# Kernel optimization log

Hardware: AMD Instinct MI355X
Metric: run time of the kernel (lower is better)

The kernel has to match this reference:

```python
import jax, jax.numpy as jnp
import numpy as np

REG = 0.01
NUM_PS, NUM_QS, NUM_RS, D = 100000, 100000, 1000, 256
B = 4096


def setup_inputs() -> dict:
    key = jax.random.key(0)
    k1, k2, k3, k4, k5, k6, k7 = jax.random.split(key, 7)
    # xavier_uniform bound for a (d, d*d) fan view: sqrt(6/(d + d*d))
    bound = float(np.sqrt(6.0 / (D + D * D)))
    return {
        "ps": jax.random.randint(k1, (B,), 0, NUM_PS),
        "qs": jax.random.randint(k2, (B,), 0, NUM_QS),
        "rs": jax.random.randint(k3, (B,), 0, NUM_RS),
        "P_table": jax.random.normal(k4, (NUM_PS, D), dtype=jnp.float32),
        "Q_table": jax.random.normal(k5, (NUM_QS, D), dtype=jnp.float32),
        "R_table": jax.random.normal(k6, (NUM_RS, D), dtype=jnp.float32),
        "W": jax.random.uniform(k7, (D, D, D), dtype=jnp.float32, minval=-bound, maxval=bound),
    }


def reference(ps, qs, rs, P_table, Q_table, R_table, W):
    p = P_table[ps]  # (B, d)
    q = Q_table[qs]  # (B, d)
    r = R_table[rs]  # (B, d)
    # W.view(d, d*d) then reshape (B, d_r, d_q): axis order of W is (p, r, q)
    # trilinear: out_b = sum_{i,j,k} p_bi W_ijk r_bj q_bk
    Wp = jnp.einsum('bi,ijk->bjk', p, W)        # (B, d, d), the big GEMM
    out = jnp.einsum('bjk,bj,bk->b', Wp, r, q)  # two batched mat-vecs
    inferences = out[:, None]                   # (B, 1)
    regs = REG * (jnp.linalg.norm(p) + jnp.linalg.norm(q) + jnp.linalg.norm(r))
    return inferences, regs
```

## Files before the change

### kernel.cpp

```cpp
#include <hip/hip_runtime.h>
#include <hip/hip_bf16.h>


#define DDIM 256
#define NIK  65536
#define BM   128
#define BN   128
#define BK   64
#define NCH2 2
#define NPANEL 8

typedef unsigned int uint;
typedef __attribute__((ext_vector_type(8))) short bf16x8;
typedef __attribute__((ext_vector_type(4))) float f32x4;

static __device__ __forceinline__ unsigned short f2bf(float f) {
    __hip_bfloat16 h = __float2bfloat16(f);
    return *reinterpret_cast<unsigned short*>(&h);
}
static __device__ __forceinline__ float bf2f(unsigned short u) {
    return __uint_as_float(((uint)u) << 16);
}

#define GLOAD_LDS16(gsrc, ldst)                                                \
    __builtin_amdgcn_global_load_lds(                                          \
        (const __attribute__((address_space(1))) void*)(gsrc),                 \
        (__attribute__((address_space(3))) void*)(ldst), 16, 0, 0)

__global__ __launch_bounds__(1024)
void fused_csr_kernel(const int* __restrict__ rs, int* __restrict__ offs,
                      int* __restrict__ list, float* __restrict__ norms,
                      int B, int n) {
    __shared__ int cnt[1024];
    __shared__ int buf[2][1024];
    const int t = threadIdx.x;
    if (t < 3) norms[t] = 0.f;
    cnt[t] = 0;
    __syncthreads();
    for (int b = t; b < B; b += 1024) atomicAdd(&cnt[rs[b]], 1);
    __syncthreads();
    const int myc = cnt[t];
    int cur = 0;
    buf[0][t] = (t < n) ? myc : 0;
    __syncthreads();
    for (int d = 1; d < 1024; d <<= 1) {
        int x = buf[cur][t] + ((t >= d) ? buf[cur][t - d] : 0);
        buf[cur ^ 1][t] = x;
        cur ^= 1;
        __syncthreads();
    }
    if (t < n) {
        int inc = buf[cur][t];
        offs[t + 1] = inc;
        if (t == 0) offs[0] = 0;
        cnt[t] = inc - myc;
    }
    __syncthreads();
    for (int b = t; b < B; b += 1024) {
        int pos = atomicAdd(&cnt[rs[b]], 1);
        list[pos] = b;
    }
}

__global__ __launch_bounds__(256)
void norm_kernel(const int* __restrict__ ps, const int* __restrict__ qs,
                 const int* __restrict__ rs, const float* __restrict__ P,
                 const float* __restrict__ Q, const float* __restrict__ R,
                 float* __restrict__ accum, int B) {
    const int which = blockIdx.y;
    const int*   idx = (which == 0) ? ps : (which == 1) ? qs : rs;
    const float* tab = (which == 0) ? P : (which == 1) ? Q : R;
    float a = 0.f;
    const int total = B * 64;
    for (int e = blockIdx.x * 256 + threadIdx.x; e < total; e += gridDim.x * 256) {
        int b = e >> 6, cc = e & 63;
        float4 v = *reinterpret_cast<const float4*>(tab + (size_t)idx[b] * DDIM + cc * 4);
        a += v.x * v.x + v.y * v.y + v.z * v.z + v.w * v.w;
    }
#pragma unroll
    for (int off = 32; off; off >>= 1) a += __shfl_down(a, off, 64);
    __shared__ float red[4];
    if ((threadIdx.x & 63) == 0) red[threadIdx.x >> 6] = a;
    __syncthreads();
    if (threadIdx.x == 0) atomicAdd(accum + which, red[0] + red[1] + red[2] + red[3]);
}

__global__ __launch_bounds__(256)
void conv_r_kernel(const float* __restrict__ R, unsigned short* __restrict__ Rb,
                   int n4) {
    int idx = blockIdx.x * 256 + threadIdx.x;
    if (idx < n4) {
        float4 v = *reinterpret_cast<const float4*>(R + idx * 4);
        ushort4 o;
        o.x = f2bf(v.x); o.y = f2bf(v.y); o.z = f2bf(v.z); o.w = f2bf(v.w);
        *reinterpret_cast<ushort4*>(Rb + idx * 4) = o;
    }
}

__global__ __launch_bounds__(256)
void conv_wt_kernel(const float* __restrict__ W, unsigned short* __restrict__ Wt) {
    const int k0 = blockIdx.x * 64;
    const int j0 = blockIdx.y * 128;
    const int i  = blockIdx.z;
    const int t  = threadIdx.x;

    __shared__ float sT[64][129];

    const float* Wi = W + (size_t)i * NIK;
#pragma unroll
    for (int it = 0; it < 8; ++it) {
        int slot = it * 256 + t;
        int jj = slot >> 4, c = slot & 15;
        float4 v = *reinterpret_cast<const float4*>(
            Wi + (size_t)(j0 + jj) * DDIM + k0 + c * 4);
        sT[c * 4 + 0][jj] = v.x;
        sT[c * 4 + 1][jj] = v.y;
        sT[c * 4 + 2][jj] = v.z;
        sT[c * 4 + 3][jj] = v.w;
    }
    __syncthreads();
#pragma unroll
    for (int it = 0; it < 4; ++it) {
        int u = it * 256 + t;
        int kk = u >> 4, jg = u & 15;
        union { unsigned short us[8]; uint4 v; } pk;
#pragma unroll
        for (int m = 0; m < 8; ++m) pk.us[m] = f2bf(sT[kk][jg * 8 + m]);
        *reinterpret_cast<uint4*>(
            Wt + (size_t)(i * DDIM + k0 + kk) * DDIM + j0 + jg * 8) = pk.v;
    }
}

__global__ __launch_bounds__(256, 2)
void stage1_kernel(const unsigned short* __restrict__ Rb,
                   const unsigned short* __restrict__ Wt,
                   unsigned short* __restrict__ WR,
                   int r_lo, int cnt) {
    const int t     = threadIdx.x;
    const int lane  = t & 63;
    const int wid   = t >> 6;
    const int strip = blockIdx.x;
    const int r0    = blockIdx.y * BM;

    __shared__ char smem[32768];

    const int wr = (wid >> 1) * 64;
    const int wn = (wid & 1) * 64;

    bf16x8 rfrag[8][4];
    {
#pragma unroll
        for (int rd = 0; rd < 4; ++rd) {
            const int j0s = rd * BK;
            __syncthreads();
#pragma unroll
            for (int c = 0; c < 4; ++c) {
                int u = c * 256 + t;
                int row = u >> 3, g = u & 7;
                int rg = r0 + row;
                if (rg >= cnt) rg = 0;
                GLOAD_LDS16(Rb + (size_t)(r_lo + rg) * DDIM + j0s +
                                ((g ^ (row & 7)) << 3),
                            smem + u * 16);
            }
            __syncthreads();
#pragma unroll
            for (int ks = 0; ks < 2; ++ks) {
                const int jg = ks * 4 + (lane >> 4);
#pragma unroll
                for (int f = 0; f < 4; ++f) {
                    int rowA = wr + f * 16 + (lane & 15);
                    rfrag[rd * 2 + ks][f] = *reinterpret_cast<const bf16x8*>(
                        smem + rowA * 128 + ((jg ^ (rowA & 7)) << 4));
                }
            }
        }
        __syncthreads();
    }

    f32x4 acc[4][4];
#pragma unroll
    for (int a = 0; a < 4; ++a)
#pragma unroll
        for (int b = 0; b < 4; ++b) {
            acc[a][b][0] = 0.f; acc[a][b][1] = 0.f;
            acc[a][b][2] = 0.f; acc[a][b][3] = 0.f;
        }

#define STAGE_W(p, kt, boff)                                                    \
    {                                                                           \
        const int j0s = (kt) * BK;                                              \
        const int n0s = strip * (BN * NPANEL) + (p) * BN;                       \
        _Pragma("unroll")                                                       \
        for (int c = 0; c < 4; ++c) {                                           \
            int u = c * 256 + t;                                                \
            int row = u >> 3, g = u & 7;                                        \
            GLOAD_LDS16(Wt + (size_t)(n0s + row) * DDIM + j0s +                 \
                            ((g ^ (row & 7)) << 3),                             \
                        smem + (boff) + u * 16);                                \
        }                                                                       \
    }

    STAGE_W(0, 0, 0);
    __syncthreads();

    const int c16   = lane & 15;
    const int gq    = lane >> 4;
    const int ubase = wn >> 5;
    char* WRb = (char*)WR;

    for (int p = 0; p < NPANEL; ++p) {
#pragma unroll
        for (int kt = 0; kt < 4; ++kt) {
            const int coff = (kt & 1) << 14;
            if (kt < 3) {
                STAGE_W(p, kt + 1, coff ^ 16384);
            } else if (p < NPANEL - 1) {
                STAGE_W(p + 1, 0, coff ^ 16384);
            }

            char* Bcur = smem + coff;
#pragma unroll
            for (int ks = 0; ks < 2; ++ks) {
                bf16x8 a[4];
                const int jg = ks * 4 + (lane >> 4);
#pragma unroll
                for (int f = 0; f < 4; ++f) {
                    int rowB = wn + f * 16 + (lane & 15);
                    a[f] = *reinterpret_cast<const bf16x8*>(
                        Bcur + rowB * 128 + ((jg ^ (rowB & 7)) << 4));
                }
#pragma unroll
                for (int fi = 0; fi < 4; ++fi)
#pragma unroll
                    for (int fr = 0; fr < 4; ++fr)
                        acc[fi][fr] = __builtin_amdgcn_mfma_f32_16x16x32_bf16(
                            a[fi], rfrag[kt * 2 + ks][fr], acc[fi][fr],
                            0, 0, 0);
            }

            if (kt == 3) {
                const int n0  = strip * (BN * NPANEL) + p * BN;
                const int i_g = n0 >> 8;
                const size_t obase = (size_t)(i_g >> 4) * 8192 +
                                     (size_t)(i_g & 15) * 512 +
                                     (size_t)(n0 & 255) * 2;
#pragma unroll
                for (int fr = 0; fr < 4; ++fr) {
                    int rg = r0 + wr + fr * 16 + c16;
                    if (rg < cnt) {
#pragma unroll
                        for (int kts = 0; kts < 2; ++kts) {
                            union { unsigned short us[8]; uint4 v; } pk;
#pragma unroll
                            for (int vv = 0; vv < 4; ++vv) {
                                pk.us[vv]     = f2bf(acc[2 * kts + 0][fr][vv]);
                                pk.us[4 + vv] = f2bf(acc[2 * kts + 1][fr][vv]);
                            }
                            *reinterpret_cast<uint4*>(
                                WRb + (size_t)rg * 131072 + obase +
                                (ubase + kts) * 64 + gq * 16) = pk.v;
                        }
                    }
                }
#pragma unroll
                for (int a2 = 0; a2 < 4; ++a2)
#pragma unroll
                    for (int b2 = 0; b2 < 4; ++b2) {
                        acc[a2][b2][0] = 0.f; acc[a2][b2][1] = 0.f;
                        acc[a2][b2][2] = 0.f; acc[a2][b2][3] = 0.f;
                    }
            }
            __syncthreads();
        }
    }
#undef STAGE_W
}

__global__ __launch_bounds__(256)
void stage2_kernel(const int* __restrict__ list, const int* __restrict__ offs,
                   const int* __restrict__ ps, const int* __restrict__ qs,
                   const float* __restrict__ P, const float* __restrict__ Q,
                   const unsigned short* __restrict__ WR,
                   float* __restrict__ partial, int r_lo, int B) {
    const int r_rel = blockIdx.x;
    const int r     = r_lo + r_rel;
    const int start = offs[r], end = offs[r + 1];
    if (start >= end) return;
    const int ihalf = blockIdx.y;
    const int t     = threadIdx.x;
    const int lane  = t & 63;
    const int w     = t >> 6;
    const int s     = lane & 15;
    const int kg    = lane >> 4;

    __shared__ float Lq[16][258];
    __shared__ float Lp[16][133];
    __shared__ float red[16][4];

    const unsigned short* Mbase = WR + (size_t)r_rel * NIK;

    for (int s0 = start; s0 < end; s0 += 16) {
        const int ns = min(16, end - s0);
        for (int u = t; u < ns * 64; u += 256) {
            int ss = u >> 6, c = u & 63;
            *reinterpret_cast<float4*>(&Lq[ss][c * 4]) =
                *reinterpret_cast<const float4*>(
                    Q + (size_t)qs[list[s0 + ss]] * DDIM + c * 4);
        }
        for (int u = t; u < ns * 32; u += 256) {
            int ss = u >> 5, c = u & 31;
            *reinterpret_cast<float4*>(&Lp[ss][c * 4]) =
                *reinterpret_cast<const float4*>(
                    P + (size_t)ps[list[s0 + ss]] * DDIM + ihalf * 128 + c * 4);
        }
        __syncthreads();

        bf16x8 bq[8];
#pragma unroll
        for (int kt = 0; kt < 8; ++kt) {
#pragma unroll
            for (int eh = 0; eh < 2; ++eh) {
#pragma unroll
                for (int ev = 0; ev < 4; ++ev) {
                    float v = (s < ns) ? Lq[s][kt * 32 + eh * 16 + kg * 4 + ev]
                                       : 0.f;
                    bq[kt][eh * 4 + ev] = (short)f2bf(v);
                }
            }
        }

        float acc_out = 0.f;
#pragma unroll
        for (int ibl = 0; ibl < 2; ++ibl) {
            const int ibh = w * 2 + ibl;
            const int ibg = ihalf * 8 + ibh;
            const unsigned short* abase =
                Mbase + (size_t)ibg * 4096 + (lane & 15) * 256 + kg * 8;
            bf16x8 af[8];
#pragma unroll
            for (int kt = 0; kt < 8; ++kt)
                af[kt] = *reinterpret_cast<const bf16x8*>(abase + kt * 32);
            f32x4 acc = {0.f, 0.f, 0.f, 0.f};
#pragma unroll
            for (int kt = 0; kt < 8; ++kt)
                acc = __builtin_amdgcn_mfma_f32_16x16x32_bf16(af[kt], bq[kt],
                                                              acc, 0, 0, 0);
#pragma unroll
            for (int reg = 0; reg < 4; ++reg) {
                int il = ibh * 16 + kg * 4 + reg;
                float pv = (s < ns) ? Lp[s][il] : 0.f;
                acc_out += acc[reg] * pv;
            }
        }
        acc_out += __shfl_xor(acc_out, 16, 64);
        acc_out += __shfl_xor(acc_out, 32, 64);
        if (lane < 16) red[s][w] = acc_out;
        __syncthreads();
        if (t < ns)
            partial[(size_t)ihalf * B + list[s0 + t]] =
                red[t][0] + red[t][1] + red[t][2] + red[t][3];
        __syncthreads();
    }
}

__global__ __launch_bounds__(256)
void sum_out_kernel(const float* __restrict__ partial,
                    const float* __restrict__ norms, float* __restrict__ out,
                    int B) {
    int b = blockIdx.x * 256 + threadIdx.x;
    if (b < B) out[b] = partial[b] + partial[(size_t)B + b];
    if (blockIdx.x == 0 && threadIdx.x == 0)
        out[B] = 0.01f * (sqrtf(norms[0]) + sqrtf(norms[1]) + sqrtf(norms[2]));
}

extern "C" void kernel_launch(void* const* d_in, const int* in_sizes, int n_in,
                              void* d_out, int out_size, void* d_ws,
                              size_t ws_size, hipStream_t stream) {
    const int*   ps = (const int*)d_in[0];
    const int*   qs = (const int*)d_in[1];
    const int*   rs = (const int*)d_in[2];
    const float* P  = (const float*)d_in[3];
    const float* Q  = (const float*)d_in[4];
    const float* R  = (const float*)d_in[5];
    const float* W  = (const float*)d_in[6];
    float* out = (float*)d_out;

    const int B      = in_sizes[0];
    const int NUM_RS = in_sizes[5] / DDIM;

    size_t off = 0;
    float* norms = (float*)((char*)d_ws + off);          off += 256;
    int* offs    = (int*)((char*)d_ws + off);            off += (size_t)(NUM_RS + 1) * 4;
    int* list    = (int*)((char*)d_ws + off);            off += (size_t)B * 4;
    off = (off + 255) & ~(size_t)255;
    float* partial = (float*)((char*)d_ws + off);        off += (size_t)NCH2 * B * 4;
    off = (off + 255) & ~(size_t)255;
    unsigned short* Rb = (unsigned short*)((char*)d_ws + off);
    off += (size_t)NUM_RS * DDIM * 2;
    off = (off + 255) & ~(size_t)255;
    unsigned short* Wt = (unsigned short*)((char*)d_ws + off);
    off += (size_t)NIK * DDIM * 2;
    off = (off + 255) & ~(size_t)255;
    unsigned short* WR = (unsigned short*)((char*)d_ws + off);

    size_t wr_bytes = (ws_size > off) ? ws_size - off : 0;
    int max_chunk = (int)(wr_bytes / ((size_t)NIK * 2));
    if (max_chunk > NUM_RS) max_chunk = NUM_RS;
    if (max_chunk < 1) max_chunk = 1;

    fused_csr_kernel<<<1, 1024, 0, stream>>>(rs, offs, list, norms, B, NUM_RS);
    norm_kernel<<<dim3(128, 3), 256, 0, stream>>>(ps, qs, rs, P, Q, R, norms, B);
    conv_r_kernel<<<(NUM_RS * DDIM / 4 + 255) / 256, 256, 0, stream>>>(
        R, Rb, NUM_RS * DDIM / 4);
    conv_wt_kernel<<<dim3(4, 2, DDIM), 256, 0, stream>>>(W, Wt);

    for (int lo = 0; lo < NUM_RS; lo += max_chunk) {
        int cnt = NUM_RS - lo;
        if (cnt > max_chunk) cnt = max_chunk;
        dim3 g1(NIK / BN / NPANEL, (cnt + BM - 1) / BM);
        stage1_kernel<<<g1, 256, 0, stream>>>(Rb, Wt, WR, lo, cnt);
        stage2_kernel<<<dim3(cnt, NCH2), 256, 0, stream>>>(
            list, offs, ps, qs, P, Q, WR, partial, lo, B);
    }
    sum_out_kernel<<<(B + 255) / 256, 256, 0, stream>>>(partial, norms, out, B);
}
```

Baseline: 119.4 us.

## Load W operand fragments directly from global memory instead of LDS double-buffering

Stage1 no longer stages W tiles through shared memory with double buffering. Each lane now reads its bf16x8 MFMA A-fragments straight from global memory, which removes the per-k-step barriers and halves LDS use, allowing higher occupancy. In exchange, each wave issues direct global loads for its fragments. Two waves share the same W rows, so data reuse now depends on cache hits, and load latency is no longer hidden by prefetching.

```diff
diff --git a/kernel.cpp b/kernel.cpp
--- a/kernel.cpp
+++ b/kernel.cpp
@@ -142,7 +142,7 @@
     const int strip = blockIdx.x;
     const int r0    = blockIdx.y * BM;
 
-    __shared__ char smem[32768];
+    __shared__ char smem[16384];
 
     const int wr = (wid >> 1) * 64;
     const int wn = (wid & 1) * 64;
@@ -175,7 +175,6 @@
                 }
             }
         }
-        __syncthreads();
     }
 
     f32x4 acc[4][4];
@@ -186,50 +185,27 @@
             acc[a][b][0] = 0.f; acc[a][b][1] = 0.f;
             acc[a][b][2] = 0.f; acc[a][b][3] = 0.f;
         }
-
-#define STAGE_W(p, kt, boff)                                                    \
-    {                                                                           \
-        const int j0s = (kt) * BK;                                              \
-        const int n0s = strip * (BN * NPANEL) + (p) * BN;                       \
-        _Pragma("unroll")                                                       \
-        for (int c = 0; c < 4; ++c) {                                           \
-            int u = c * 256 + t;                                                \
-            int row = u >> 3, g = u & 7;                                        \
-            GLOAD_LDS16(Wt + (size_t)(n0s + row) * DDIM + j0s +                 \
-                            ((g ^ (row & 7)) << 3),                             \
-                        smem + (boff) + u * 16);                                \
-        }                                                                       \
-    }
-
-    STAGE_W(0, 0, 0);
-    __syncthreads();
 
     const int c16   = lane & 15;
     const int gq    = lane >> 4;
     const int ubase = wn >> 5;
     char* WRb = (char*)WR;
 
+    const unsigned short* WtL =
+        Wt + (size_t)(strip * (BN * NPANEL) + wn + c16) * DDIM + gq * 8;
+
     for (int p = 0; p < NPANEL; ++p) {
+        const unsigned short* WtP = WtL + (size_t)p * BN * DDIM;
 #pragma unroll
         for (int kt = 0; kt < 4; ++kt) {
-            const int coff = (kt & 1) << 14;
-            if (kt < 3) {
-                STAGE_W(p, kt + 1, coff ^ 16384);
-            } else if (p < NPANEL - 1) {
-                STAGE_W(p + 1, 0, coff ^ 16384);
-            }
-
-            char* Bcur = smem + coff;
 #pragma unroll
             for (int ks = 0; ks < 2; ++ks) {
+                const int joff = (kt * 2 + ks) * 32;
                 bf16x8 a[4];
-                const int jg = ks * 4 + (lane >> 4);
-#pragma unroll
-                for (int f = 0; f < 4; ++f) {
-                    int rowB = wn + f * 16 + (lane & 15);
+#pragma unroll
+                for (int f = 0; f < 4; ++f)
                     a[f] = *reinterpret_cast<const bf16x8*>(
-                        Bcur + rowB * 128 + ((jg ^ (rowB & 7)) << 4));
-                }
+                        WtP + (size_t)(f * 16) * DDIM + joff);
 #pragma unroll
                 for (int fi = 0; fi < 4; ++fi)
 #pragma unroll
@@ -238,43 +214,40 @@
                             a[fi], rfrag[kt * 2 + ks][fr], acc[fi][fr],
                             0, 0, 0);
             }
-
-            if (kt == 3) {
-                const int n0  = strip * (BN * NPANEL) + p * BN;
-                const int i_g = n0 >> 8;
-                const size_t obase = (size_t)(i_g >> 4) * 8192 +
-                                     (size_t)(i_g & 15) * 512 +
-                                     (size_t)(n0 & 255) * 2;
-#pragma unroll
-                for (int fr = 0; fr < 4; ++fr) {
-                    int rg = r0 + wr + fr * 16 + c16;
-                    if (rg < cnt) {
-#pragma unroll
-                        for (int kts = 0; kts < 2; ++kts) {
-                            union { unsigned short us[8]; uint4 v; } pk;
-#pragma unroll
-                            for (int vv = 0; vv < 4; ++vv) {
-                                pk.us[vv]     = f2bf(acc[2 * kts + 0][fr][vv]);
-                                pk.us[4 + vv] = f2bf(acc[2 * kts + 1][fr][vv]);
-                            }
-                            *reinterpret_cast<uint4*>(
-                                WRb + (size_t)rg * 131072 + obase +
-                                (ubase + kts) * 64 + gq * 16) = pk.v;
+        }
+        {
+            const int n0  = strip * (BN * NPANEL) + p * BN;
+            const int i_g = n0 >> 8;
+            const size_t obase = (size_t)(i_g >> 4) * 8192 +
+                                 (size_t)(i_g & 15) * 512 +
+                                 (size_t)(n0 & 255) * 2;
+#pragma unroll
+            for (int fr = 0; fr < 4; ++fr) {
+                int rg = r0 + wr + fr * 16 + c16;
+                if (rg < cnt) {
+#pragma unroll
+                    for (int kts = 0; kts < 2; ++kts) {
+                        union { unsigned short us[8]; uint4 v; } pk;
+#pragma unroll
+                        for (int vv = 0; vv < 4; ++vv) {
+                            pk.us[vv]     = f2bf(acc[2 * kts + 0][fr][vv]);
+                            pk.us[4 + vv] = f2bf(acc[2 * kts + 1][fr][vv]);
                         }
+                        *reinterpret_cast<uint4*>(
+                            WRb + (size_t)rg * 131072 + obase +
+                            (ubase + kts) * 64 + gq * 16) = pk.v;
                     }
                 }
-#pragma unroll
-                for (int a2 = 0; a2 < 4; ++a2)
-#pragma unroll
-                    for (int b2 = 0; b2 < 4; ++b2) {
-                        acc[a2][b2][0] = 0.f; acc[a2][b2][1] = 0.f;
-                        acc[a2][b2][2] = 0.f; acc[a2][b2][3] = 0.f;
-                    }
-            }
-            __syncthreads();
-        }
-    }
-#undef STAGE_W
+            }
+#pragma unroll
+            for (int a2 = 0; a2 < 4; ++a2)
+#pragma unroll
+                for (int b2 = 0; b2 < 4; ++b2) {
+                    acc[a2][b2][0] = 0.f; acc[a2][b2][1] = 0.f;
+                    acc[a2][b2][2] = 0.f; acc[a2][b2][3] = 0.f;
+                }
+        }
+    }
 }
 
 __global__ __launch_bounds__(256)
```

Measured after the change: 144.3 us. 1.21x slower.

## Double K-step W staging in stage1 and fold R conversion into norm kernel

Applied to the files above, without the earlier changes.

Stage1 now stages two K-tiles of the W panel per barrier into a 64KB LDS double buffer, which halves the number of __syncthreads per panel and gives each prefetch more MFMA work to hide behind. Separately, the R-table bf16 conversion moves into an extra grid row of the norm kernel, removing one kernel launch. Doubling LDS to 64KB may lower occupancy below the two blocks per CU requested by the launch bounds, and the larger prefetch raises register and LDS pressure.

```diff
diff --git a/kernel.cpp b/kernel.cpp
--- a/kernel.cpp
+++ b/kernel.cpp
@@ -66,13 +66,24 @@
 void norm_kernel(const int* __restrict__ ps, const int* __restrict__ qs,
                  const int* __restrict__ rs, const float* __restrict__ P,
                  const float* __restrict__ Q, const float* __restrict__ R,
-                 float* __restrict__ accum, int B) {
+                 unsigned short* __restrict__ Rb, float* __restrict__ accum,
+                 int B, int n4) {
     const int which = blockIdx.y;
+    if (which == 3) {
+        for (int idx = blockIdx.x * 256 + threadIdx.x; idx < n4;
+             idx += 128 * 256) {
+            float4 v = *reinterpret_cast<const float4*>(R + idx * 4);
+            ushort4 o;
+            o.x = f2bf(v.x); o.y = f2bf(v.y); o.z = f2bf(v.z); o.w = f2bf(v.w);
+            *reinterpret_cast<ushort4*>(Rb + idx * 4) = o;
+        }
+        return;
+    }
     const int*   idx = (which == 0) ? ps : (which == 1) ? qs : rs;
     const float* tab = (which == 0) ? P : (which == 1) ? Q : R;
     float a = 0.f;
     const int total = B * 64;
-    for (int e = blockIdx.x * 256 + threadIdx.x; e < total; e += gridDim.x * 256) {
+    for (int e = blockIdx.x * 256 + threadIdx.x; e < total; e += 128 * 256) {
         int b = e >> 6, cc = e & 63;
         float4 v = *reinterpret_cast<const float4*>(tab + (size_t)idx[b] * DDIM + cc * 4);
         a += v.x * v.x + v.y * v.y + v.z * v.z + v.w * v.w;
@@ -83,18 +94,6 @@
     if ((threadIdx.x & 63) == 0) red[threadIdx.x >> 6] = a;
     __syncthreads();
     if (threadIdx.x == 0) atomicAdd(accum + which, red[0] + red[1] + red[2] + red[3]);
-}
-
-__global__ __launch_bounds__(256)
-void conv_r_kernel(const float* __restrict__ R, unsigned short* __restrict__ Rb,
-                   int n4) {
-    int idx = blockIdx.x * 256 + threadIdx.x;
-    if (idx < n4) {
-        float4 v = *reinterpret_cast<const float4*>(R + idx * 4);
-        ushort4 o;
-        o.x = f2bf(v.x); o.y = f2bf(v.y); o.z = f2bf(v.z); o.w = f2bf(v.w);
-        *reinterpret_cast<ushort4*>(Rb + idx * 4) = o;
-    }
 }
 
 __global__ __launch_bounds__(256)
@@ -142,7 +141,7 @@
     const int strip = blockIdx.x;
     const int r0    = blockIdx.y * BM;
 
-    __shared__ char smem[32768];
+    __shared__ char smem[65536];
 
     const int wr = (wid >> 1) * 64;
     const int wn = (wid & 1) * 64;
@@ -187,10 +186,10 @@
             acc[a][b][2] = 0.f; acc[a][b][3] = 0.f;
         }
 
-#define STAGE_W(p, kt, boff)                                                    \
+#define STAGE_W1(ktg, boff)                                                     \
     {                                                                           \
-        const int j0s = (kt) * BK;                                              \
-        const int n0s = strip * (BN * NPANEL) + (p) * BN;                       \
+        const int j0s = ((ktg) & 3) * BK;                                       \
+        const int n0s = strip * (BN * NPANEL) + ((ktg) >> 2) * BN;              \
         _Pragma("unroll")                                                       \
         for (int c = 0; c < 4; ++c) {                                           \
             int u = c * 256 + t;                                                \
@@ -201,7 +200,8 @@
         }                                                                       \
     }
 
-    STAGE_W(0, 0, 0);
+    STAGE_W1(0, 0);
+    STAGE_W1(1, 16384);
     __syncthreads();
 
     const int c16   = lane & 15;
@@ -211,35 +211,41 @@
 
     for (int p = 0; p < NPANEL; ++p) {
 #pragma unroll
-        for (int kt = 0; kt < 4; ++kt) {
-            const int coff = (kt & 1) << 14;
-            if (kt < 3) {
-                STAGE_W(p, kt + 1, coff ^ 16384);
-            } else if (p < NPANEL - 1) {
-                STAGE_W(p + 1, 0, coff ^ 16384);
-            }
-
-            char* Bcur = smem + coff;
-#pragma unroll
-            for (int ks = 0; ks < 2; ++ks) {
-                bf16x8 a[4];
-                const int jg = ks * 4 + (lane >> 4);
-#pragma unroll
-                for (int f = 0; f < 4; ++f) {
-                    int rowB = wn + f * 16 + (lane & 15);
-                    a[f] = *reinterpret_cast<const bf16x8*>(
-                        Bcur + rowB * 128 + ((jg ^ (rowB & 7)) << 4));
+        for (int dh = 0; dh < 2; ++dh) {
+            const int d    = p * 2 + dh;
+            const int coff = dh << 15;
+            const int noff = coff ^ 32768;
+            if (d < 15) {
+                STAGE_W1(2 * d + 2, noff);
+                STAGE_W1(2 * d + 3, noff + 16384);
+            }
+
+#pragma unroll
+            for (int j = 0; j < 2; ++j) {
+                const int kt = dh * 2 + j;
+                char* Bcur = smem + coff + (j << 14);
+#pragma unroll
+                for (int ks = 0; ks < 2; ++ks) {
+                    bf16x8 a[4];
+                    const int jg = ks * 4 + (lane >> 4);
+#pragma unroll
+                    for (int f = 0; f < 4; ++f) {
+                        int rowB = wn + f * 16 + (lane & 15);
+                        a[f] = *reinterpret_cast<const bf16x8*>(
+                            Bcur + rowB * 128 + ((jg ^ (rowB & 7)) << 4));
+                    }
+#pragma unroll
+                    for (int fi = 0; fi < 4; ++fi)
+#pragma unroll
+                        for (int fr = 0; fr < 4; ++fr)
+                            acc[fi][fr] =
+                                __builtin_amdgcn_mfma_f32_16x16x32_bf16(
+                                    a[fi], rfrag[kt * 2 + ks][fr],
+                                    acc[fi][fr], 0, 0, 0);
                 }
-#pragma unroll
-                for (int fi = 0; fi < 4; ++fi)
-#pragma unroll
-                    for (int fr = 0; fr < 4; ++fr)
-                        acc[fi][fr] = __builtin_amdgcn_mfma_f32_16x16x32_bf16(
-                            a[fi], rfrag[kt * 2 + ks][fr], acc[fi][fr],
-                            0, 0, 0);
-            }
-
-            if (kt == 3) {
+            }
+
+            if (dh == 1) {
                 const int n0  = strip * (BN * NPANEL) + p * BN;
                 const int i_g = n0 >> 8;
                 const size_t obase = (size_t)(i_g >> 4) * 8192 +
@@ -274,7 +280,7 @@
             __syncthreads();
         }
     }
-#undef STAGE_W
+#undef STAGE_W1
 }
 
 __global__ __launch_bounds__(256)
@@ -410,9 +416,8 @@
     if (max_chunk < 1) max_chunk = 1;
 
     fused_csr_kernel<<<1, 1024, 0, stream>>>(rs, offs, list, norms, B, NUM_RS);
-    norm_kernel<<<dim3(128, 3), 256, 0, stream>>>(ps, qs, rs, P, Q, R, norms, B);
-    conv_r_kernel<<<(NUM_RS * DDIM / 4 + 255) / 256, 256, 0, stream>>>(
-        R, Rb, NUM_RS * DDIM / 4);
+    norm_kernel<<<dim3(128, 4), 256, 0, stream>>>(ps, qs, rs, P, Q, R, Rb,
+                                                  norms, B, NUM_RS * DDIM / 4);
     conv_wt_kernel<<<dim3(4, 2, DDIM), 256, 0, stream>>>(W, Wt);
 
     for (int lo = 0; lo < NUM_RS; lo += max_chunk) {
```

Result: no change. 118.4 us (median of 2 runs) (-0.8%).

## Defer stage1 output stores into next panel and fuse R conversion into norm kernel

Applied to the files above, without the earlier changes.

Stage1 now packs each panel's bf16 results into registers and writes them out during the next panel's MFMA loop instead of at the panel end. Its __syncthreads calls become explicit vmcnt waits plus s_barrier so the pending global stores can stay in flight. Out-of-range rows are clamped to a spare row rather than branched around, which is why max_chunk reserves one extra row. The R-to-bf16 conversion is folded into norm_kernel as a fourth grid slice to save a launch. The cost is register pressure from the pending buffer and more complex wait-count logic.

```diff
diff --git a/kernel.cpp b/kernel.cpp
--- a/kernel.cpp
+++ b/kernel.cpp
@@ -66,13 +66,24 @@
 void norm_kernel(const int* __restrict__ ps, const int* __restrict__ qs,
                  const int* __restrict__ rs, const float* __restrict__ P,
                  const float* __restrict__ Q, const float* __restrict__ R,
-                 float* __restrict__ accum, int B) {
+                 unsigned short* __restrict__ Rb, float* __restrict__ accum,
+                 int B, int n4) {
     const int which = blockIdx.y;
+    if (which == 3) {
+        for (int idx = blockIdx.x * 256 + threadIdx.x; idx < n4;
+             idx += 128 * 256) {
+            float4 v = *reinterpret_cast<const float4*>(R + idx * 4);
+            ushort4 o;
+            o.x = f2bf(v.x); o.y = f2bf(v.y); o.z = f2bf(v.z); o.w = f2bf(v.w);
+            *reinterpret_cast<ushort4*>(Rb + idx * 4) = o;
+        }
+        return;
+    }
     const int*   idx = (which == 0) ? ps : (which == 1) ? qs : rs;
     const float* tab = (which == 0) ? P : (which == 1) ? Q : R;
     float a = 0.f;
     const int total = B * 64;
-    for (int e = blockIdx.x * 256 + threadIdx.x; e < total; e += gridDim.x * 256) {
+    for (int e = blockIdx.x * 256 + threadIdx.x; e < total; e += 128 * 256) {
         int b = e >> 6, cc = e & 63;
         float4 v = *reinterpret_cast<const float4*>(tab + (size_t)idx[b] * DDIM + cc * 4);
         a += v.x * v.x + v.y * v.y + v.z * v.z + v.w * v.w;
@@ -83,18 +94,6 @@
     if ((threadIdx.x & 63) == 0) red[threadIdx.x >> 6] = a;
     __syncthreads();
     if (threadIdx.x == 0) atomicAdd(accum + which, red[0] + red[1] + red[2] + red[3]);
-}
-
-__global__ __launch_bounds__(256)
-void conv_r_kernel(const float* __restrict__ R, unsigned short* __restrict__ Rb,
-                   int n4) {
-    int idx = blockIdx.x * 256 + threadIdx.x;
-    if (idx < n4) {
-        float4 v = *reinterpret_cast<const float4*>(R + idx * 4);
-        ushort4 o;
-        o.x = f2bf(v.x); o.y = f2bf(v.y); o.z = f2bf(v.z); o.w = f2bf(v.w);
-        *reinterpret_cast<ushort4*>(Rb + idx * 4) = o;
-    }
 }
 
 __global__ __launch_bounds__(256)
@@ -202,21 +201,37 @@
     }
 
     STAGE_W(0, 0, 0);
-    __syncthreads();
+    asm volatile("s_waitcnt vmcnt(0)" ::: "memory");
+    __builtin_amdgcn_sched_barrier(0);
+    __builtin_amdgcn_s_barrier();
+    __builtin_amdgcn_sched_barrier(0);
 
     const int c16   = lane & 15;
     const int gq    = lane >> 4;
     const int ubase = wn >> 5;
     char* WRb = (char*)WR;
 
+    uint4  pend[8];
+    size_t pobase = 0;
+
     for (int p = 0; p < NPANEL; ++p) {
 #pragma unroll
         for (int kt = 0; kt < 4; ++kt) {
-            const int coff = (kt & 1) << 14;
+            const int  coff = (kt & 1) << 14;
+            const bool last = (p == NPANEL - 1) && (kt == 3);
+
             if (kt < 3) {
                 STAGE_W(p, kt + 1, coff ^ 16384);
             } else if (p < NPANEL - 1) {
                 STAGE_W(p + 1, 0, coff ^ 16384);
+            }
+
+            if (p > 0) {
+                int rg  = r0 + wr + kt * 16 + c16;
+                int rgc = rg < cnt ? rg : cnt;
+                char* sp = WRb + (size_t)rgc * 131072 + pobase + gq * 16;
+                *reinterpret_cast<uint4*>(sp + ubase * 64)       = pend[2 * kt];
+                *reinterpret_cast<uint4*>(sp + (ubase + 1) * 64) = pend[2 * kt + 1];
             }
 
             char* Bcur = smem + coff;
@@ -242,25 +257,20 @@
             if (kt == 3) {
                 const int n0  = strip * (BN * NPANEL) + p * BN;
                 const int i_g = n0 >> 8;
-                const size_t obase = (size_t)(i_g >> 4) * 8192 +
-                                     (size_t)(i_g & 15) * 512 +
-                                     (size_t)(n0 & 255) * 2;
+                pobase = (size_t)(i_g >> 4) * 8192 +
+                         (size_t)(i_g & 15) * 512 +
+                         (size_t)(n0 & 255) * 2;
 #pragma unroll
                 for (int fr = 0; fr < 4; ++fr) {
-                    int rg = r0 + wr + fr * 16 + c16;
-                    if (rg < cnt) {
-#pragma unroll
-                        for (int kts = 0; kts < 2; ++kts) {
-                            union { unsigned short us[8]; uint4 v; } pk;
-#pragma unroll
-                            for (int vv = 0; vv < 4; ++vv) {
-                                pk.us[vv]     = f2bf(acc[2 * kts + 0][fr][vv]);
-                                pk.us[4 + vv] = f2bf(acc[2 * kts + 1][fr][vv]);
-                            }
-                            *reinterpret_cast<uint4*>(
-                                WRb + (size_t)rg * 131072 + obase +
-                                (ubase + kts) * 64 + gq * 16) = pk.v;
+#pragma unroll
+                    for (int kts = 0; kts < 2; ++kts) {
+                        union { unsigned short us[8]; uint4 v; } pk;
+#pragma unroll
+                        for (int vv = 0; vv < 4; ++vv) {
+                            pk.us[vv]     = f2bf(acc[2 * kts + 0][fr][vv]);
+                            pk.us[4 + vv] = f2bf(acc[2 * kts + 1][fr][vv]);
                         }
+                        pend[fr * 2 + kts] = pk.v;
                     }
                 }
 #pragma unroll
@@ -271,8 +281,27 @@
                         acc[a2][b2][2] = 0.f; acc[a2][b2][3] = 0.f;
                     }
             }
-            __syncthreads();
-        }
+
+            if (!last) {
+                if (p > 0) {
+                    asm volatile("s_waitcnt vmcnt(2)" ::: "memory");
+                } else {
+                    asm volatile("s_waitcnt vmcnt(0)" ::: "memory");
+                }
+                __builtin_amdgcn_sched_barrier(0);
+                __builtin_amdgcn_s_barrier();
+                __builtin_amdgcn_sched_barrier(0);
+            }
+        }
+    }
+
+#pragma unroll
+    for (int kt = 0; kt < 4; ++kt) {
+        int rg  = r0 + wr + kt * 16 + c16;
+        int rgc = rg < cnt ? rg : cnt;
+        char* sp = WRb + (size_t)rgc * 131072 + pobase + gq * 16;
+        *reinterpret_cast<uint4*>(sp + ubase * 64)       = pend[2 * kt];
+        *reinterpret_cast<uint4*>(sp + (ubase + 1) * 64) = pend[2 * kt + 1];
     }
 #undef STAGE_W
 }
@@ -405,14 +434,13 @@
     unsigned short* WR = (unsigned short*)((char*)d_ws + off);
 
     size_t wr_bytes = (ws_size > off) ? ws_size - off : 0;
-    int max_chunk = (int)(wr_bytes / ((size_t)NIK * 2));
+    int max_chunk = (int)(wr_bytes / ((size_t)NIK * 2)) - 1;
     if (max_chunk > NUM_RS) max_chunk = NUM_RS;
     if (max_chunk < 1) max_chunk = 1;
 
     fused_csr_kernel<<<1, 1024, 0, stream>>>(rs, offs, list, norms, B, NUM_RS);
-    norm_kernel<<<dim3(128, 3), 256, 0, stream>>>(ps, qs, rs, P, Q, R, norms, B);
-    conv_r_kernel<<<(NUM_RS * DDIM / 4 + 255) / 256, 256, 0, stream>>>(
-        R, Rb, NUM_RS * DDIM / 4);
+    norm_kernel<<<dim3(128, 4), 256, 0, stream>>>(ps, qs, rs, P, Q, R, Rb,
+                                                  norms, B, NUM_RS * DDIM / 4);
     conv_wt_kernel<<<dim3(4, 2, DDIM), 256, 0, stream>>>(W, Wt);
 
     for (int lo = 0; lo < NUM_RS; lo += max_chunk) {
```

New measurement: 170.8 us. +43.1%, slower.
